# Performance work log

Hardware: AMD Instinct MI355X
Metric: run time of the kernel (lower is better)

Reference implementation:

```python
import jax, jax.numpy as jnp
import numpy as np

D = 256
N = 1024
L = 6
H = 4
NAMES = ['self', 'cross', 'self', 'cross', 'self', 'cross']


def setup_inputs() -> dict:
    key = jax.random.key(0)
    ks = jax.random.split(key, 12)
    f32 = jnp.float32
    s = D ** -0.5
    s2 = (2 * D) ** -0.5
    return {
        'desc0': jax.random.normal(ks[0], (1, D, N), f32),
        'desc1': jax.random.normal(ks[1], (1, D, N), f32),
        'desc2': jax.random.normal(ks[2], (1, D, N), f32),
        'desc3': jax.random.normal(ks[3], (1, D, N), f32),
        'dist': jax.random.uniform(ks[4], (1, N, N), f32),
        'unreachable': jnp.zeros((N, N), dtype=bool),
        'fidx': jax.random.randint(ks[5], (N, 2), 0, 100),
        'lmb': jax.random.randint(ks[6], (8, 4), 0, 100),
        'proj_w': jax.random.normal(ks[7], (3, L, 3, D, D), f32) * s,
        'proj_b': jnp.zeros((3, L, 3, D), f32),
        'merge_w': jax.random.normal(ks[8], (3, L, D, D), f32) * s,
        'merge_b': jnp.zeros((3, L, D), f32),
        'mlp_w1': jax.random.normal(ks[9], (3, L, 2 * D, 2 * D), f32) * s2,
        'mlp_b1': jnp.zeros((3, L, 2 * D), f32),
        'mlp_w2': jax.random.normal(ks[10], (3, L, D, 2 * D), f32) * s2,
        'mlp_b2': jnp.zeros((3, L, D), f32),
        'norm_g': jnp.ones((4, L, D), f32),
        'norm_b': jnp.zeros((4, L, D), f32),
    }


def _conv(w, b, x):
    # Conv1d kernel_size=1 == per-position linear over channel dim. x: [1, Cin, N]
    return jnp.einsum('od,bdn->bon', w, x) + b[None, :, None]


def _ln(x, g, b):
    # torch does LayerNorm(D) on x.transpose(1,2); equivalent to normalizing channel dim of [1, D, N]
    mu = jnp.mean(x, axis=1, keepdims=True)
    var = jnp.var(x, axis=1, keepdims=True)
    xn = (x - mu) * jax.lax.rsqrt(var + 1e-5)
    return xn * g[None, :, None] + b[None, :, None]


def _mha(pw, pb, mw, mb, q, k, v):
    # pw: [3, D, D], pb: [3, D]; q/k/v: [1, D, Nq/Nk/Nk]; mask is always None in this model
    dh = D // H
    qh = _conv(pw[0], pb[0], q).reshape(1, dh, H, -1)  # [1, dh, H, Nq]
    kh = _conv(pw[1], pb[1], k).reshape(1, dh, H, -1)
    vh = _conv(pw[2], pb[2], v).reshape(1, dh, H, -1)
    scores = jnp.einsum('bdhn,bdhm->bhnm', qh, kh) / jnp.asarray(dh, q.dtype) ** 0.5
    prob = jax.nn.softmax(scores, axis=-1)
    x = jnp.einsum('bhnm,bdhm->bdhn', prob, vh)  # [1, dh, H, Nq]
    out = _conv(mw, mb, x.reshape(1, D, -1))
    return out, scores.mean(axis=1)  # weights: [1, Nq, Nk]


def reference(desc0, desc1, desc2, desc3, dist, unreachable, fidx, lmb,
              proj_w, proj_b, merge_w, merge_b, mlp_w1, mlp_b1, mlp_w2, mlp_b2,
              norm_g, norm_b):
    # ablation == 0 path; dist, fidx, lmb feed dead code in the original forward.
    def prop(br, i, x, src):
        msg, wts = _mha(proj_w[br, i], proj_b[br, i], merge_w[br, i], merge_b[br, i], x, src, src)
        h = jnp.concatenate([x, msg], axis=1)  # [1, 2D, N]
        h = jax.nn.relu(_conv(mlp_w1[br, i], mlp_b1[br, i], h))
        return _conv(mlp_w2[br, i], mlp_b2[br, i], h), wts

    d0, d1, d2, d3 = desc0, desc1, desc2, desc3
    score1 = None
    for i, name in enumerate(NAMES):
        if name == 'cross':
            src0, src1 = d1, d0
        else:
            src0, src1 = d0, d1
        delta0, _ = prop(0, i, d0, src0)
        delta1, score1 = prop(0, i, d1, src1)
        if name == 'cross':
            delta21, _ = prop(1, i, d2, d1)
            delta12, _ = prop(1, i, d1, d2)
            d2 = _ln(d2 + delta21, norm_g[2, i], norm_b[2, i])
            delta03, _ = prop(2, i, d0, d3)
            delta30, _ = prop(2, i, d3, d0)
            d3 = _ln(d3 + delta30, norm_g[3, i], norm_b[3, i])
            d0 = d0 + delta0 + delta03
            d1 = d1 + delta1 + delta12
        else:
            delta2, _ = prop(1, i, d2, d2)
            d2 = _ln(d2 + delta2, norm_g[2, i], norm_b[2, i])
            delta3, _ = prop(2, i, d3, d3)
            d3 = _ln(d3 + delta3, norm_g[3, i], norm_b[3, i])
            d0 = d0 + delta0
            d1 = d1 + delta1
        d0 = _ln(d0, norm_g[0, i], norm_b[0, i])
        d1 = _ln(d1, norm_g[1, i], norm_b[1, i])

    scores = score1.mean(axis=1).reshape(-1)  # [N0]
    unreachable_frontiers = jnp.any(unreachable, axis=0)  # [N0]
    return jnp.where(unreachable_frontiers, jnp.asarray(-1e9, scores.dtype), scores)
```

## Files before the change

### kernel.cpp

```cpp
#include <hip/hip_runtime.h>

#define D 256
#define NPTS 1024
#define H 4
#define LNUM 6

static constexpr size_t SL = (size_t)D * NPTS;

typedef __attribute__((ext_vector_type(8))) short bf16x8;
typedef __attribute__((ext_vector_type(4))) float f32x4;

__device__ __forceinline__ unsigned f2bf(float f) {
  unsigned u = __float_as_uint(f);
  return (u + 0x7FFFu + ((u >> 16) & 1u)) >> 16;
}
__device__ __forceinline__ unsigned pack2(float a, float b) {
  return f2bf(a) | (f2bf(b) << 16);
}
__device__ __forceinline__ float bf2f(unsigned u) {
  return __uint_as_float(u << 16);
}
__device__ __forceinline__ int swz(int row, int byteInRow) {
  return row * 128 + (byteInRow ^ ((row & 7) << 4));
}

struct MMArgs {
  const unsigned short* X[18];
  const unsigned short* X2[18];
  const unsigned short* W[18];
  const float* B[18];
  void* O[18];
};

template <bool RELU>
__global__ __launch_bounds__(256) void mm_bf16(MMArgs a, int K, int xs, int os,
                                               int mode0, int qkv, int split) {
  const int z = blockIdx.z;
  const unsigned short* __restrict__ X = a.X[z];
  const unsigned short* __restrict__ X2 = a.X2[z];
  const unsigned short* __restrict__ W = a.W[z];
  const float* __restrict__ Bb = a.B[z];

  int mode = mode0, osz = os;
  if (qkv && (z % 3 == 2)) { mode = 2; osz = 1024; }

  __shared__ char sm[64 * 68 * 4];
  char* smX = sm;
  char* smW = sm + 8192;

  const int tid = threadIdx.x;
  const int n0 = blockIdx.x * 64, m0 = blockIdx.y * 64;
  const int lane = tid & 63, wid = tid >> 6;

  f32x4 acc[4] = {{0.f, 0.f, 0.f, 0.f}, {0.f, 0.f, 0.f, 0.f},
                  {0.f, 0.f, 0.f, 0.f}, {0.f, 0.f, 0.f, 0.f}};

  const int srow = tid >> 3, skb = (tid & 7) * 16;
  const int ar = wid * 16 + (lane & 15);
  const int kh = (lane >> 4) * 16;

  for (int k0 = 0; k0 < K; k0 += 64) {
    const int kw = k0 + (skb >> 1);
    int kx = kw;
    const unsigned short* xsrc = X;
    if (split && kx >= split) { xsrc = X2; kx -= split; }
#pragma unroll
    for (int p = 0; p < 2; ++p) {
      const int row = srow + 32 * p;
      *(float4*)(smX + swz(row, skb)) =
          *(const float4*)(xsrc + (size_t)(n0 + row) * xs + kx);
      *(float4*)(smW + swz(row, skb)) =
          *(const float4*)(W + (size_t)(m0 + row) * K + kw);
    }
    __syncthreads();
    const bf16x8 a0 = *(const bf16x8*)(smX + swz(ar, kh));
    const bf16x8 a1 = *(const bf16x8*)(smX + swz(ar, 64 + kh));
#pragma unroll
    for (int c = 0; c < 4; ++c) {
      const int br = c * 16 + (lane & 15);
      const bf16x8 b0 = *(const bf16x8*)(smW + swz(br, kh));
      const bf16x8 b1 = *(const bf16x8*)(smW + swz(br, 64 + kh));
      acc[c] = __builtin_amdgcn_mfma_f32_16x16x32_bf16(a0, b0, acc[c], 0, 0, 0);
      acc[c] = __builtin_amdgcn_mfma_f32_16x16x32_bf16(a1, b1, acc[c], 0, 0, 0);
    }
    __syncthreads();
  }

  float(*eps)[68] = (float(*)[68])sm;
#pragma unroll
  for (int c = 0; c < 4; ++c) {
    const float bs = Bb[m0 + c * 16 + (lane & 15)];
#pragma unroll
    for (int r = 0; r < 4; ++r) {
      float v = acc[c][r] + bs;
      if (RELU) v = fmaxf(v, 0.f);
      eps[wid * 16 + (lane >> 4) * 4 + r][c * 16 + (lane & 15)] = v;
    }
  }
  __syncthreads();

#pragma unroll
  for (int p = 0; p < 2; ++p) {
    const int row = srow + 32 * p;
    const int c0 = (tid & 7) * 8;
    if (mode == 0) {
      const float4 lo = *(const float4*)&eps[row][c0];
      const float4 hi = *(const float4*)&eps[row][c0 + 4];
      uint4 u = {pack2(lo.x, lo.y), pack2(lo.z, lo.w), pack2(hi.x, hi.y), pack2(hi.z, hi.w)};
      *(uint4*)((unsigned short*)a.O[z] + (size_t)(n0 + row) * osz + m0 + c0) = u;
    } else if (mode == 1) {
      float* O = (float*)a.O[z];
      *(float4*)(O + (size_t)(n0 + row) * osz + m0 + c0) = *(const float4*)&eps[row][c0];
      *(float4*)(O + (size_t)(n0 + row) * osz + m0 + c0 + 4) = *(const float4*)&eps[row][c0 + 4];
    } else {
      float v[8];
#pragma unroll
      for (int j = 0; j < 8; ++j) v[j] = eps[c0 + j][row];
      uint4 u = {pack2(v[0], v[1]), pack2(v[2], v[3]), pack2(v[4], v[5]), pack2(v[6], v[7])};
      *(uint4*)((unsigned short*)a.O[z] + (size_t)(m0 + row) * osz + n0 + c0) = u;
    }
  }
}

struct AttnArgs {
  const unsigned short* Q[6];
  const unsigned short* K[6];
  const unsigned short* V[6];
};

__global__ __launch_bounds__(256) void attn_split(AttnArgs a, unsigned short* part) {
  const int z = blockIdx.z;
  const int h = blockIdx.y >> 2, ck = blockIdx.y & 3;
  const int n0 = blockIdx.x * 64;
  const unsigned short* __restrict__ Qp = a.Q[z];
  const unsigned short* __restrict__ Kp = a.K[z];
  const unsigned short* __restrict__ Vp = a.V[z];

  __shared__ char sm[49152];
  char* smQ = sm;
  char* smKb = sm + 8192;
  char* smVb = sm + 24576;
  char* smP = sm + 40960;

  const int tid = threadIdx.x;
  const int lane = tid & 63, wid = tid >> 6;
  const int srow = tid >> 2, skb = (tid & 3) * 16;
  const int kb0 = ck * 256;

#pragma unroll
  for (int p = 0; p < 2; ++p) {
    const int b = skb + 64 * p;
    *(float4*)(smQ + swz(srow, b)) =
        *(const float4*)(Qp + (size_t)(n0 + srow) * 256 + h * 64 + (b >> 1));
    *(float4*)(smKb + swz(srow, b)) =
        *(const float4*)(Kp + (size_t)(kb0 + srow) * 256 + h * 64 + (b >> 1));
    *(float4*)(smVb + swz(srow, b)) =
        *(const float4*)(Vp + (size_t)(h * 64 + srow) * NPTS + kb0 + (b >> 1));
  }
  __syncthreads();

  const int ar = wid * 16 + (lane & 15);
  const int kh = (lane >> 4) * 16;
  const bf16x8 qa0 = *(const bf16x8*)(smQ + swz(ar, kh));
  const bf16x8 qa1 = *(const bf16x8*)(smQ + swz(ar, 64 + kh));

  f32x4 accO[4] = {{0.f, 0.f, 0.f, 0.f}, {0.f, 0.f, 0.f, 0.f},
                   {0.f, 0.f, 0.f, 0.f}, {0.f, 0.f, 0.f, 0.f}};
  float mrun[4] = {-1e30f, -1e30f, -1e30f, -1e30f};
  float lrun[4] = {0.f, 0.f, 0.f, 0.f};

  for (int t = 0; t < 4; ++t) {
    const int co = (t & 1) << 13;
    if (t < 3) {
      const int no = ((t + 1) & 1) << 13;
      const int kt = kb0 + (t + 1) * 64;
#pragma unroll
      for (int p = 0; p < 2; ++p) {
        const int b = skb + 64 * p;
        *(float4*)(smKb + no + swz(srow, b)) =
            *(const float4*)(Kp + (size_t)(kt + srow) * 256 + h * 64 + (b >> 1));
        *(float4*)(smVb + no + swz(srow, b)) =
            *(const float4*)(Vp + (size_t)(h * 64 + srow) * NPTS + kt + (b >> 1));
      }
    }

    f32x4 s[4];
#pragma unroll
    for (int c = 0; c < 4; ++c) {
      const int br = c * 16 + (lane & 15);
      const bf16x8 kf0 = *(const bf16x8*)(smKb + co + swz(br, kh));
      const bf16x8 kf1 = *(const bf16x8*)(smKb + co + swz(br, 64 + kh));
      f32x4 tt = {0.f, 0.f, 0.f, 0.f};
      tt = __builtin_amdgcn_mfma_f32_16x16x32_bf16(qa0, kf0, tt, 0, 0, 0);
      tt = __builtin_amdgcn_mfma_f32_16x16x32_bf16(qa1, kf1, tt, 0, 0, 0);
      s[c] = tt * 0.125f;
    }

#pragma unroll
    for (int r = 0; r < 4; ++r) {
      float mx = fmaxf(fmaxf(s[0][r], s[1][r]), fmaxf(s[2][r], s[3][r]));
#pragma unroll
      for (int o = 1; o < 16; o <<= 1) mx = fmaxf(mx, __shfl_xor(mx, o));
      const float mn = fmaxf(mrun[r], mx);
      const float corr = __expf(mrun[r] - mn);
      mrun[r] = mn;
      float ps = 0.f;
#pragma unroll
      for (int c = 0; c < 4; ++c) {
        const float e = __expf(s[c][r] - mn);
        s[c][r] = e;
        ps += e;
      }
#pragma unroll
      for (int o = 1; o < 16; o <<= 1) ps += __shfl_xor(ps, o);
      lrun[r] = lrun[r] * corr + ps;
#pragma unroll
      for (int c = 0; c < 4; ++c) accO[c][r] *= corr;
    }

#pragma unroll
    for (int c = 0; c < 4; ++c)
#pragma unroll
      for (int r = 0; r < 4; ++r) {
        const float p0 = s[c][r];
        const float p1 = __shfl_xor(p0, 1);
        if (!(lane & 1)) {
          const int row = wid * 16 + (lane >> 4) * 4 + r;
          const int ktb = (c * 16 + (lane & 15)) * 2;
          *(unsigned*)(smP + swz(row, ktb)) = pack2(p0, p1);
        }
      }

    const bf16x8 pa0 = *(const bf16x8*)(smP + swz(ar, kh));
    const bf16x8 pa1 = *(const bf16x8*)(smP + swz(ar, 64 + kh));
#pragma unroll
    for (int c = 0; c < 4; ++c) {
      const int vr = c * 16 + (lane & 15);
      const bf16x8 vb0 = *(const bf16x8*)(smVb + co + swz(vr, kh));
      const bf16x8 vb1 = *(const bf16x8*)(smVb + co + swz(vr, 64 + kh));
      accO[c] = __builtin_amdgcn_mfma_f32_16x16x32_bf16(pa0, vb0, accO[c], 0, 0, 0);
      accO[c] = __builtin_amdgcn_mfma_f32_16x16x32_bf16(pa1, vb1, accO[c], 0, 0, 0);
    }
    __syncthreads();
  }

  char* rec = (char*)part +
              (size_t)((((z * 4 + h) * 16 + blockIdx.x) * 4 + ck)) * 8704;
#pragma unroll
  for (int c = 0; c < 4; ++c)
#pragma unroll
    for (int r = 0; r < 4; ++r) {
      const float o0 = accO[c][r];
      const float o1 = __shfl_xor(o0, 1);
      if (!(lane & 1)) {
        const int row = wid * 16 + (lane >> 4) * 4 + r;
        const int col = c * 16 + (lane & 15);
        *(unsigned*)(rec + row * 128 + col * 2) = pack2(o0, o1);
      }
    }
  if ((lane & 15) == 0) {
#pragma unroll
    for (int r = 0; r < 4; ++r) {
      const int row = wid * 16 + (lane >> 4) * 4 + r;
      *(float*)(rec + 8192 + row * 4) = mrun[r];
      *(float*)(rec + 8448 + row * 4) = lrun[r];
    }
  }
}

struct CmbArgs {
  unsigned short* O[6];
};

__global__ __launch_bounds__(256) void attn_combine(CmbArgs a,
                                                    const unsigned short* part) {
  const int z = blockIdx.z, h = blockIdx.y, qb = blockIdx.x;
  const int tid = threadIdx.x;
  const int q = tid >> 2, t4 = tid & 3;
  const char* base = (const char*)part + (size_t)(((z * 4 + h) * 16 + qb) * 4) * 8704;

  float m[4], l[4];
#pragma unroll
  for (int i = 0; i < 4; ++i) {
    m[i] = *(const float*)(base + i * 8704 + 8192 + q * 4);
    l[i] = *(const float*)(base + i * 8704 + 8448 + q * 4);
  }
  const float M = fmaxf(fmaxf(m[0], m[1]), fmaxf(m[2], m[3]));
  float w[4], L = 0.f;
#pragma unroll
  for (int i = 0; i < 4; ++i) { w[i] = __expf(m[i] - M); L += w[i] * l[i]; }
  const float invL = 1.f / L;

  float o[16] = {};
#pragma unroll
  for (int i = 0; i < 4; ++i) {
    const char* Or = base + i * 8704 + q * 128 + t4 * 32;
    unsigned ua[8];
    *(uint4*)ua = *(const uint4*)Or;
    *(uint4*)(ua + 4) = *(const uint4*)(Or + 16);
#pragma unroll
    for (int j = 0; j < 8; ++j) {
      o[2 * j] += w[i] * bf2f(ua[j] & 0xFFFFu);
      o[2 * j + 1] += w[i] * bf2f(ua[j] >> 16);
    }
  }
  unsigned ou[8];
#pragma unroll
  for (int j = 0; j < 8; ++j) ou[j] = pack2(o[2 * j] * invL, o[2 * j + 1] * invL);
  unsigned short* Op = a.O[z] + (size_t)(qb * 64 + q) * 256 + h * 64 + t4 * 16;
  *(uint4*)Op = *(uint4*)ou;
  *(uint4*)(Op + 8) = *(uint4*)(ou + 4);
}

struct LnArgs {
  float* x[4];
  unsigned short* xb[4];
  const float* da[4];
  const float* db[4];
  const float* g[4];
  const float* b[4];
};

__global__ __launch_bounds__(256) void ln_rows(LnArgs a) {
  const int z = blockIdx.z;
  float* __restrict__ x = a.x[z];
  unsigned short* __restrict__ xb = a.xb[z];
  const float* __restrict__ da = a.da[z];
  const float* __restrict__ db = a.db[z];
  const float* __restrict__ g = a.g[z];
  const float* __restrict__ b = a.b[z];

  const int lane = threadIdx.x & 63, wid = threadIdx.x >> 6;
  const int n = blockIdx.x * 4 + wid;
  const size_t off = (size_t)n * 256 + lane * 4;

  float4 v = *(const float4*)(x + off);
  if (da) {
    const float4 w = *(const float4*)(da + off);
    v.x += w.x; v.y += w.y; v.z += w.z; v.w += w.w;
  }
  if (db) {
    const float4 w = *(const float4*)(db + off);
    v.x += w.x; v.y += w.y; v.z += w.z; v.w += w.w;
  }
  float s = v.x + v.y + v.z + v.w;
  float q = v.x * v.x + v.y * v.y + v.z * v.z + v.w * v.w;
#pragma unroll
  for (int o = 1; o < 64; o <<= 1) {
    s += __shfl_xor(s, o);
    q += __shfl_xor(q, o);
  }
  const float mu = s * (1.f / 256.f);
  const float var = q * (1.f / 256.f) - mu * mu;
  const float inv = rsqrtf(var + 1e-5f);
  const float4 gv = *(const float4*)(g + lane * 4);
  const float4 bv = *(const float4*)(b + lane * 4);
  float4 o;
  o.x = (v.x - mu) * inv * gv.x + bv.x;
  o.y = (v.y - mu) * inv * gv.y + bv.y;
  o.z = (v.z - mu) * inv * gv.z + bv.z;
  o.w = (v.w - mu) * inv * gv.w + bv.w;
  *(float4*)(x + off) = o;
  uint2 pk = {pack2(o.x, o.y), pack2(o.z, o.w)};
  *(uint2*)(xb + off) = pk;
}

struct TrArgs {
  const float* s[4];
  float* d[4];
  unsigned short* db[4];
};
__global__ __launch_bounds__(256) void tr_init(TrArgs a) {
  const int z = blockIdx.z;
  const int n0 = blockIdx.x * 64, c0 = blockIdx.y * 64;
  __shared__ float T[64][65];
  const int tid = threadIdx.x;
#pragma unroll
  for (int p = 0; p < 4; ++p) {
    const int row = (tid >> 4) + 16 * p;
    const int col4 = (tid & 15) * 4;
    const float4 v = *(const float4*)(a.s[z] + (size_t)(c0 + row) * NPTS + n0 + col4);
    T[row][col4] = v.x; T[row][col4 + 1] = v.y; T[row][col4 + 2] = v.z; T[row][col4 + 3] = v.w;
  }
  __syncthreads();
#pragma unroll
  for (int p = 0; p < 4; ++p) {
    const int nr = (tid >> 4) + 16 * p;
    const int c4 = (tid & 15) * 4;
    float4 v;
    v.x = T[c4][nr]; v.y = T[c4 + 1][nr]; v.z = T[c4 + 2][nr]; v.w = T[c4 + 3][nr];
    *(float4*)(a.d[z] + (size_t)(n0 + nr) * 256 + c0 + c4) = v;
    uint2 pk = {pack2(v.x, v.y), pack2(v.z, v.w)};
    *(uint2*)(a.db[z] + (size_t)(n0 + nr) * 256 + c0 + c4) = pk;
  }
}

__global__ __launch_bounds__(256) void wp_qkv(const float* __restrict__ pw,
                                              const float* __restrict__ pb,
                                              unsigned short* __restrict__ wbf,
                                              float* __restrict__ pbias) {
  const int z = blockIdx.z;
  const int pi = z / 3, j = z % 3;
  const int br = pi / 5, i = pi % 5;
  const float* src = pw + (((size_t)br * LNUM + i) * 3 + j) * 65536;
  unsigned short* dst = wbf + (size_t)pi * 655360 + (size_t)j * 65536;
  const int t = blockIdx.x * 256 + threadIdx.x;
  const int mp = t >> 6, k4 = (t & 63) * 4;
  const int m = (mp & 63) * 4 + (mp >> 6);
  const float4 v = *(const float4*)(src + (size_t)m * 256 + k4);
  uint2 pk = {pack2(v.x, v.y), pack2(v.z, v.w)};
  *(uint2*)(dst + (size_t)mp * 256 + k4) = pk;
  if (blockIdx.x == 0) {
    const float* sb = pb + (((size_t)br * LNUM + i) * 3 + j) * 256;
    const int mb = threadIdx.x;
    pbias[(size_t)z * 256 + mb] = sb[(mb & 63) * 4 + (mb >> 6)];
  }
}

__global__ __launch_bounds__(256) void wp_mw(const float* __restrict__ mw,
                                             unsigned short* __restrict__ wbf) {
  const int pi = blockIdx.z;
  const int br = pi / 5, i = pi % 5;
  const float* src = mw + ((size_t)br * LNUM + i) * 65536;
  unsigned short* dst = wbf + (size_t)pi * 655360 + 196608;
  const int t = blockIdx.x * 256 + threadIdx.x;
  const int m = t >> 6, c4 = (t & 63) * 4;
  float v[4];
#pragma unroll
  for (int u = 0; u < 4; ++u) {
    const int cp = c4 + u;
    v[u] = src[(size_t)m * 256 + (cp & 63) * 4 + (cp >> 6)];
  }
  uint2 pk = {pack2(v[0], v[1]), pack2(v[2], v[3])};
  *(uint2*)(dst + (size_t)m * 256 + c4) = pk;
}

__global__ __launch_bounds__(256) void wp_c1(const float* __restrict__ w1,
                                             unsigned short* __restrict__ wbf) {
  const int pi = blockIdx.z;
  const int br = pi / 5, i = pi % 5;
  const float* src = w1 + ((size_t)br * LNUM + i) * 262144;
  unsigned short* dst = wbf + (size_t)pi * 655360 + 262144;
  const int t = blockIdx.x * 256 + threadIdx.x;
  const float4 v = *(const float4*)(src + (size_t)t * 4);
  uint2 pk = {pack2(v.x, v.y), pack2(v.z, v.w)};
  *(uint2*)(dst + (size_t)t * 4) = pk;
}

__global__ __launch_bounds__(256) void wp_c2(const float* __restrict__ w2,
                                             unsigned short* __restrict__ wbf) {
  const int pi = blockIdx.z;
  const int br = pi / 5, i = pi % 5;
  const float* src = w2 + ((size_t)br * LNUM + i) * 131072;
  unsigned short* dst = wbf + (size_t)pi * 655360 + 524288;
  const int t = blockIdx.x * 256 + threadIdx.x;
  const float4 v = *(const float4*)(src + (size_t)t * 4);
  uint2 pk = {pack2(v.x, v.y), pack2(v.z, v.w)};
  *(uint2*)(dst + (size_t)t * 4) = pk;
}

__device__ __forceinline__ float block_reduce_sum(float v) {
  __shared__ float smr[4];
  const int lane = threadIdx.x & 63, wid = threadIdx.x >> 6;
#pragma unroll
  for (int off = 32; off; off >>= 1) v += __shfl_xor(v, off);
  if (lane == 0) smr[wid] = v;
  __syncthreads();
  if (threadIdx.x == 0) v = smr[0] + smr[1] + smr[2] + smr[3];
  return v;
}

__global__ __launch_bounds__(256) void cs1(const float* __restrict__ X,
                                           float* __restrict__ part) {
  const int r0 = blockIdx.x * 64;
  float acc = 0.f;
  for (int r = 0; r < 64; ++r) acc += X[(size_t)(r0 + r) * 256 + threadIdx.x];
  part[(size_t)blockIdx.x * 256 + threadIdx.x] = acc;
}
__global__ __launch_bounds__(256) void cs2(const float* __restrict__ part,
                                           float* __restrict__ s1) {
  float acc = 0.f;
  for (int b = 0; b < 16; ++b) acc += part[(size_t)b * 256 + threadIdx.x];
  s1[threadIdx.x] = acc;
}
__global__ __launch_bounds__(256) void matvec_qbar(const float* __restrict__ Wq,
                                                   const float* __restrict__ bq,
                                                   const float* __restrict__ s1,
                                                   float* __restrict__ qbar) {
  const int d = blockIdx.x, t = threadIdx.x;
  float s = Wq[(size_t)d * 256 + t] * s1[t];
  s = block_reduce_sum(s);
  if (t == 0) qbar[d] = s + (float)NPTS * bq[d];
}
__global__ __launch_bounds__(256) void matvec_u(const float* __restrict__ Wk,
                                                const float* __restrict__ bk,
                                                const float* __restrict__ qbar,
                                                float* __restrict__ u) {
  const int c = blockIdx.x, t = threadIdx.x;
  float s = (c < 256) ? (Wk[(size_t)t * 256 + c] * qbar[t]) : (bk[t] * qbar[t]);
  s = block_reduce_sum(s);
  if (t == 0) u[c] = s;
}

__global__ __launch_bounds__(256) void ur_or(const unsigned* __restrict__ U,
                                             unsigned* __restrict__ part) {
  const int b = blockIdx.x;
  unsigned o = 0;
  for (int r = 0; r < 16; ++r) o |= U[(size_t)(b * 16 + r) * 256 + threadIdx.x];
  part[(size_t)b * 256 + threadIdx.x] = o;
}

__global__ __launch_bounds__(256) void final2(const float* __restrict__ d0,
                                              const float* __restrict__ u,
                                              const unsigned* __restrict__ part,
                                              float* __restrict__ out) {
  const int lane = threadIdx.x & 63, wid = threadIdx.x >> 6;
  const int m = blockIdx.x * 4 + wid;
  const float4 v = *(const float4*)(d0 + (size_t)m * 256 + lane * 4);
  const float4 uu = *(const float4*)(u + lane * 4);
  float s = v.x * uu.x + v.y * uu.y + v.z * uu.z + v.w * uu.w;
  unsigned f = part[(size_t)lane * 256 + (m >> 2)];
  f = (f >> ((m & 3) * 8)) & 0xFFu;
#pragma unroll
  for (int o = 32; o; o >>= 1) {
    s += __shfl_xor(s, o);
    f |= (unsigned)__shfl_xor((int)f, o);
  }
  if (lane == 0) out[m] = f ? -1e9f : (s + u[256]) * (1.f / 32768.f);
}

extern "C" void kernel_launch(void* const* d_in, const int* in_sizes, int n_in,
                              void* d_out, int out_size, void* d_ws, size_t ws_size,
                              hipStream_t stream) {
  const float* desc[4] = {(const float*)d_in[0], (const float*)d_in[1],
                          (const float*)d_in[2], (const float*)d_in[3]};
  const unsigned char* unreach = (const unsigned char*)d_in[5];
  const float* proj_w = (const float*)d_in[8];
  const float* proj_b = (const float*)d_in[9];
  const float* merge_w = (const float*)d_in[10];
  const float* merge_b = (const float*)d_in[11];
  const float* mlp_w1 = (const float*)d_in[12];
  const float* mlp_b1 = (const float*)d_in[13];
  const float* mlp_w2 = (const float*)d_in[14];
  const float* mlp_b2 = (const float*)d_in[15];
  const float* norm_g = (const float*)d_in[16];
  const float* norm_b = (const float*)d_in[17];
  float* out = (float*)d_out;

  float* ws = (float*)d_ws;
  float* dbufF[4];
  for (int t = 0; t < 4; ++t) dbufF[t] = ws + (size_t)t * SL;
  unsigned short* dbfB[4];
  for (int t = 0; t < 4; ++t) dbfB[t] = (unsigned short*)(ws + 4 * SL) + (size_t)t * SL;
  float* deltaF[6];
  for (int p = 0; p < 6; ++p) deltaF[p] = ws + 6 * SL + (size_t)p * SL;
  unsigned short* wbf = (unsigned short*)(ws + 12 * SL);
  float* pbias = ws + 12 * SL + 4915200;
  unsigned* urpart = (unsigned*)(pbias + 11520);
  float* cspart = pbias + 11520 + 16384;
  float* s1 = cspart + 4096;
  float* qbar = s1 + 256;
  float* uvec = qbar + 256;
  unsigned short* attnpart = (unsigned short*)(ws + 12 * SL + 4915200 + 32832);
  const size_t base_f = 12 * SL + 4915200 + 32832 + 3342336;
  long long avail = (long long)(ws_size / 4) - (long long)base_f;
  const size_t SET_US = 5 * SL;
  int nsets = (int)(avail / (long long)(SET_US / 2));
  if (nsets > 6) nsets = 6;
  if (nsets < 1) nsets = 1;
  unsigned short* usBase = (unsigned short*)(ws + base_f);
  auto setQ = [&](int p) { return usBase + (size_t)p * SET_US; };
  auto setK = [&](int p) { return usBase + (size_t)p * SET_US + SL; };
  auto setV = [&](int p) { return usBase + (size_t)p * SET_US + 2 * SL; };
  auto setO = [&](int p) { return usBase + (size_t)p * SET_US + 3 * SL; };
  auto setM = [&](int p) { return usBase + (size_t)p * SET_US + 4 * SL; };
  auto setH1 = [&](int p) { return usBase + (size_t)p * SET_US; };

  ur_or<<<dim3(64), 256, 0, stream>>>((const unsigned*)unreach, urpart);
  wp_qkv<<<dim3(64, 1, 45), 256, 0, stream>>>(proj_w, proj_b, wbf, pbias);
  wp_mw<<<dim3(64, 1, 15), 256, 0, stream>>>(merge_w, wbf);
  wp_c1<<<dim3(256, 1, 15), 256, 0, stream>>>(mlp_w1, wbf);
  wp_c2<<<dim3(128, 1, 15), 256, 0, stream>>>(mlp_w2, wbf);
  {
    TrArgs ta{};
    for (int t = 0; t < 4; ++t) { ta.s[t] = desc[t]; ta.d[t] = dbufF[t]; ta.db[t] = dbfB[t]; }
    tr_init<<<dim3(16, 4, 4), 256, 0, stream>>>(ta);
  }

  static const int selfp[4][3] = {{0, 0, 0}, {0, 1, 1}, {1, 2, 2}, {2, 3, 3}};
  static const int crossp[6][3] = {{0, 0, 1}, {0, 1, 0}, {1, 2, 1},
                                   {1, 1, 2}, {2, 0, 3}, {2, 3, 0}};

  for (int i = 0; i < 5; ++i) {
    const bool cross = (i & 1);
    const int np = cross ? 6 : 4;
    const int(*props)[3] = cross ? crossp : selfp;

    for (int p0 = 0; p0 < np; p0 += nsets) {
      const int g = (np - p0 < nsets) ? (np - p0) : nsets;

      {
        MMArgs m{};
        for (int p = 0; p < g; ++p) {
          const int br = props[p0 + p][0], xi = props[p0 + p][1], si = props[p0 + p][2];
          const int pi = br * 5 + i;
          unsigned short* wb = wbf + (size_t)pi * 655360;
          const unsigned short* xq = dbfB[xi];
          const unsigned short* xsv = dbfB[si];
          m.X[p * 3 + 0] = xq; m.X2[p * 3 + 0] = xq; m.W[p * 3 + 0] = wb;
          m.B[p * 3 + 0] = pbias + ((size_t)pi * 3 + 0) * 256; m.O[p * 3 + 0] = setQ(p);
          m.X[p * 3 + 1] = xsv; m.X2[p * 3 + 1] = xsv; m.W[p * 3 + 1] = wb + 65536;
          m.B[p * 3 + 1] = pbias + ((size_t)pi * 3 + 1) * 256; m.O[p * 3 + 1] = setK(p);
          m.X[p * 3 + 2] = xsv; m.X2[p * 3 + 2] = xsv; m.W[p * 3 + 2] = wb + 131072;
          m.B[p * 3 + 2] = pbias + ((size_t)pi * 3 + 2) * 256; m.O[p * 3 + 2] = setV(p);
        }
        mm_bf16<false><<<dim3(16, 4, 3 * g), 256, 0, stream>>>(m, 256, 256, 256, 0, 1, 0);
      }
      {
        AttnArgs aa{};
        for (int p = 0; p < g; ++p) {
          aa.Q[p] = setQ(p); aa.K[p] = setK(p); aa.V[p] = setV(p);
        }
        attn_split<<<dim3(16, 16, g), 256, 0, stream>>>(aa, attnpart);
        CmbArgs cc{};
        for (int p = 0; p < g; ++p) cc.O[p] = setO(p);
        attn_combine<<<dim3(16, 4, g), 256, 0, stream>>>(cc, attnpart);
      }
      {
        MMArgs m{};
        for (int p = 0; p < g; ++p) {
          const int br = props[p0 + p][0];
          const int pi = br * 5 + i;
          m.X[p] = setO(p); m.X2[p] = setO(p);
          m.W[p] = wbf + (size_t)pi * 655360 + 196608;
          m.B[p] = merge_b + ((size_t)br * LNUM + i) * 256; m.O[p] = setM(p);
        }
        mm_bf16<false><<<dim3(16, 4, g), 256, 0, stream>>>(m, 256, 256, 256, 0, 0, 0);
      }
      {
        MMArgs m{};
        for (int p = 0; p < g; ++p) {
          const int br = props[p0 + p][0], xi = props[p0 + p][1];
          const int pi = br * 5 + i;
          m.X[p] = dbfB[xi]; m.X2[p] = setM(p);
          m.W[p] = wbf + (size_t)pi * 655360 + 262144;
          m.B[p] = mlp_b1 + ((size_t)br * LNUM + i) * 512; m.O[p] = setH1(p);
        }
        mm_bf16<true><<<dim3(16, 8, g), 256, 0, stream>>>(m, 512, 256, 512, 0, 0, 256);
      }
      {
        MMArgs m{};
        for (int p = 0; p < g; ++p) {
          const int br = props[p0 + p][0];
          const int pi = br * 5 + i;
          m.X[p] = setH1(p); m.X2[p] = setH1(p);
          m.W[p] = wbf + (size_t)pi * 655360 + 524288;
          m.B[p] = mlp_b2 + ((size_t)br * LNUM + i) * 256; m.O[p] = deltaF[p0 + p];
        }
        mm_bf16<false><<<dim3(16, 4, g), 256, 0, stream>>>(m, 512, 512, 256, 1, 0, 0);
      }
    }

    {
      LnArgs la{};
      for (int t = 0; t < 4; ++t) {
        la.x[t] = dbufF[t]; la.xb[t] = dbfB[t];
        const float* da = nullptr;
        const float* db2 = nullptr;
        for (int p = 0; p < np; ++p)
          if (props[p][1] == t) {
            if (!da) da = deltaF[p];
            else db2 = deltaF[p];
          }
        la.da[t] = da; la.db[t] = db2;
        la.g[t] = norm_g + ((size_t)t * LNUM + i) * 256;
        la.b[t] = norm_b + ((size_t)t * LNUM + i) * 256;
      }
      ln_rows<<<dim3(256, 1, 4), 256, 0, stream>>>(la);
    }
  }

  const float* Wq5 = proj_w + (((size_t)0 * LNUM + 5) * 3 + 0) * 65536;
  const float* bq5 = proj_b + (((size_t)0 * LNUM + 5) * 3 + 0) * 256;
  const float* Wk5 = proj_w + (((size_t)0 * LNUM + 5) * 3 + 1) * 65536;
  const float* bk5 = proj_b + (((size_t)0 * LNUM + 5) * 3 + 1) * 256;

  cs1<<<dim3(16), 256, 0, stream>>>(dbufF[1], cspart);
  cs2<<<dim3(1), 256, 0, stream>>>(cspart, s1);
  matvec_qbar<<<dim3(256), 256, 0, stream>>>(Wq5, bq5, s1, qbar);
  matvec_u<<<dim3(257), 256, 0, stream>>>(Wk5, bk5, qbar, uvec);
  final2<<<dim3(256), 256, 0, stream>>>(dbufF[0], uvec, urpart, out);

  (void)in_sizes; (void)n_in; (void)out_size;
}
```

Measured before the change: 388.0 us.

## Fold merge projection into MLP first layer and transpose attention score layout

The merge conv weight is pre-multiplied into the second half of the MLP first-layer weight, and the merge bias is folded into a new first-layer bias, so each propagation drops one GEMM launch and one intermediate buffer. The 1/sqrt(dh) scale moves into the Q projection epilogue. The attention kernel computes S transposed so each lane owns one query row, which removes the 16-lane shuffle reductions and the per-element shuffle when writing P. Folding the merge weights changes bf16 rounding because the fused product is itself rounded to bf16.

```diff
diff --git a/kernel.cpp b/kernel.cpp
--- a/kernel.cpp
+++ b/kernel.cpp
@@ -43,6 +43,7 @@
 
   int mode = mode0, osz = os;
   if (qkv && (z % 3 == 2)) { mode = 2; osz = 1024; }
+  const float osc = (qkv && (z % 3 == 0)) ? 0.125f : 1.0f;
 
   __shared__ char sm[64 * 68 * 4];
   char* smX = sm;
@@ -92,7 +93,7 @@
     const float bs = Bb[m0 + c * 16 + (lane & 15)];
 #pragma unroll
     for (int r = 0; r < 4; ++r) {
-      float v = acc[c][r] + bs;
+      float v = (acc[c][r] + bs) * osc;
       if (RELU) v = fmaxf(v, 0.f);
       eps[wid * 16 + (lane >> 4) * 4 + r][c * 16 + (lane & 15)] = v;
     }
@@ -159,15 +160,14 @@
   }
   __syncthreads();
 
-  const int ar = wid * 16 + (lane & 15);
   const int kh = (lane >> 4) * 16;
-  const bf16x8 qa0 = *(const bf16x8*)(smQ + swz(ar, kh));
-  const bf16x8 qa1 = *(const bf16x8*)(smQ + swz(ar, 64 + kh));
+  const int qr = wid * 16 + (lane & 15);
+  const bf16x8 qb0 = *(const bf16x8*)(smQ + swz(qr, kh));
+  const bf16x8 qb1 = *(const bf16x8*)(smQ + swz(qr, 64 + kh));
 
   f32x4 accO[4] = {{0.f, 0.f, 0.f, 0.f}, {0.f, 0.f, 0.f, 0.f},
                    {0.f, 0.f, 0.f, 0.f}, {0.f, 0.f, 0.f, 0.f}};
-  float mrun[4] = {-1e30f, -1e30f, -1e30f, -1e30f};
-  float lrun[4] = {0.f, 0.f, 0.f, 0.f};
+  float mrun = -1e30f, lrun = 0.f;
 
   for (int t = 0; t < 4; ++t) {
     const int co = (t & 1) << 13;
@@ -191,48 +191,51 @@
       const bf16x8 kf0 = *(const bf16x8*)(smKb + co + swz(br, kh));
       const bf16x8 kf1 = *(const bf16x8*)(smKb + co + swz(br, 64 + kh));
       f32x4 tt = {0.f, 0.f, 0.f, 0.f};
-      tt = __builtin_amdgcn_mfma_f32_16x16x32_bf16(qa0, kf0, tt, 0, 0, 0);
-      tt = __builtin_amdgcn_mfma_f32_16x16x32_bf16(qa1, kf1, tt, 0, 0, 0);
-      s[c] = tt * 0.125f;
-    }
-
-#pragma unroll
-    for (int r = 0; r < 4; ++r) {
-      float mx = fmaxf(fmaxf(s[0][r], s[1][r]), fmaxf(s[2][r], s[3][r]));
-#pragma unroll
-      for (int o = 1; o < 16; o <<= 1) mx = fmaxf(mx, __shfl_xor(mx, o));
-      const float mn = fmaxf(mrun[r], mx);
-      const float corr = __expf(mrun[r] - mn);
-      mrun[r] = mn;
-      float ps = 0.f;
-#pragma unroll
-      for (int c = 0; c < 4; ++c) {
+      tt = __builtin_amdgcn_mfma_f32_16x16x32_bf16(kf0, qb0, tt, 0, 0, 0);
+      tt = __builtin_amdgcn_mfma_f32_16x16x32_bf16(kf1, qb1, tt, 0, 0, 0);
+      s[c] = tt;
+    }
+
+    float mx = s[0][0];
+#pragma unroll
+    for (int c = 0; c < 4; ++c)
+#pragma unroll
+      for (int r = 0; r < 4; ++r) mx = fmaxf(mx, s[c][r]);
+    mx = fmaxf(mx, __shfl_xor(mx, 16));
+    mx = fmaxf(mx, __shfl_xor(mx, 32));
+    const float mn = fmaxf(mrun, mx);
+    const float corr = __expf(mrun - mn);
+    mrun = mn;
+    float ps = 0.f;
+#pragma unroll
+    for (int c = 0; c < 4; ++c)
+#pragma unroll
+      for (int r = 0; r < 4; ++r) {
         const float e = __expf(s[c][r] - mn);
         s[c][r] = e;
         ps += e;
       }
-#pragma unroll
-      for (int o = 1; o < 16; o <<= 1) ps += __shfl_xor(ps, o);
-      lrun[r] = lrun[r] * corr + ps;
-#pragma unroll
-      for (int c = 0; c < 4; ++c) accO[c][r] *= corr;
-    }
-
-#pragma unroll
-    for (int c = 0; c < 4; ++c)
-#pragma unroll
-      for (int r = 0; r < 4; ++r) {
-        const float p0 = s[c][r];
-        const float p1 = __shfl_xor(p0, 1);
-        if (!(lane & 1)) {
-          const int row = wid * 16 + (lane >> 4) * 4 + r;
-          const int ktb = (c * 16 + (lane & 15)) * 2;
-          *(unsigned*)(smP + swz(row, ktb)) = pack2(p0, p1);
-        }
-      }
-
-    const bf16x8 pa0 = *(const bf16x8*)(smP + swz(ar, kh));
-    const bf16x8 pa1 = *(const bf16x8*)(smP + swz(ar, 64 + kh));
+    ps += __shfl_xor(ps, 16);
+    ps += __shfl_xor(ps, 32);
+    lrun = lrun * corr + ps;
+
+#pragma unroll
+    for (int c = 0; c < 4; ++c) {
+      uint2 u;
+      u.x = pack2(s[c][0], s[c][1]);
+      u.y = pack2(s[c][2], s[c][3]);
+      *(uint2*)(smP + swz(qr, c * 32 + (lane >> 4) * 8)) = u;
+    }
+
+#pragma unroll
+    for (int r = 0; r < 4; ++r) {
+      const float cr = __shfl(corr, ((lane >> 4) & 3) * 4 + r);
+#pragma unroll
+      for (int c = 0; c < 4; ++c) accO[c][r] *= cr;
+    }
+
+    const bf16x8 pa0 = *(const bf16x8*)(smP + swz(qr, kh));
+    const bf16x8 pa1 = *(const bf16x8*)(smP + swz(qr, 64 + kh));
 #pragma unroll
     for (int c = 0; c < 4; ++c) {
       const int vr = c * 16 + (lane & 15);
@@ -258,13 +261,9 @@
         *(unsigned*)(rec + row * 128 + col * 2) = pack2(o0, o1);
       }
     }
-  if ((lane & 15) == 0) {
-#pragma unroll
-    for (int r = 0; r < 4; ++r) {
-      const int row = wid * 16 + (lane >> 4) * 4 + r;
-      *(float*)(rec + 8192 + row * 4) = mrun[r];
-      *(float*)(rec + 8448 + row * 4) = lrun[r];
-    }
+  if (lane < 16) {
+    *(float*)(rec + 8192 + (wid * 16 + lane) * 4) = mrun;
+    *(float*)(rec + 8448 + (wid * 16 + lane) * 4) = lrun;
   }
 }
 
@@ -417,26 +416,27 @@
   }
 }
 
-__global__ __launch_bounds__(256) void wp_mw(const float* __restrict__ mw,
-                                             unsigned short* __restrict__ wbf) {
+__global__ __launch_bounds__(256) void wp_mwt(const float* __restrict__ mw,
+                                              unsigned short* __restrict__ wbf,
+                                              float* __restrict__ zb) {
   const int pi = blockIdx.z;
   const int br = pi / 5, i = pi % 5;
   const float* src = mw + ((size_t)br * LNUM + i) * 65536;
   unsigned short* dst = wbf + (size_t)pi * 655360 + 196608;
   const int t = blockIdx.x * 256 + threadIdx.x;
-  const int m = t >> 6, c4 = (t & 63) * 4;
+  const int cp = t >> 6, m4 = (t & 63) * 4;
+  const int c = (cp & 63) * 4 + (cp >> 6);
   float v[4];
 #pragma unroll
-  for (int u = 0; u < 4; ++u) {
-    const int cp = c4 + u;
-    v[u] = src[(size_t)m * 256 + (cp & 63) * 4 + (cp >> 6)];
-  }
+  for (int u = 0; u < 4; ++u) v[u] = src[(size_t)(m4 + u) * 256 + c];
   uint2 pk = {pack2(v[0], v[1]), pack2(v[2], v[3])};
-  *(uint2*)(dst + (size_t)m * 256 + c4) = pk;
+  *(uint2*)(dst + (size_t)cp * 256 + m4) = pk;
+  if (blockIdx.x == 0 && pi == 0) zb[threadIdx.x] = 0.f;
 }
 
 __global__ __launch_bounds__(256) void wp_c1(const float* __restrict__ w1,
-                                             unsigned short* __restrict__ wbf) {
+                                             unsigned short* __restrict__ wbf,
+                                             unsigned short* __restrict__ whi) {
   const int pi = blockIdx.z;
   const int br = pi / 5, i = pi % 5;
   const float* src = w1 + ((size_t)br * LNUM + i) * 262144;
@@ -445,6 +445,9 @@
   const float4 v = *(const float4*)(src + (size_t)t * 4);
   uint2 pk = {pack2(v.x, v.y), pack2(v.z, v.w)};
   *(uint2*)(dst + (size_t)t * 4) = pk;
+  const int idx = t * 4, row = idx >> 9, col = idx & 511;
+  if (col >= 256)
+    *(uint2*)(whi + (size_t)pi * 131072 + (size_t)row * 256 + (col - 256)) = pk;
 }
 
 __global__ __launch_bounds__(256) void wp_c2(const float* __restrict__ w2,
@@ -457,6 +460,27 @@
   const float4 v = *(const float4*)(src + (size_t)t * 4);
   uint2 pk = {pack2(v.x, v.y), pack2(v.z, v.w)};
   *(uint2*)(dst + (size_t)t * 4) = pk;
+}
+
+__global__ __launch_bounds__(256) void b1fold(const float* __restrict__ w1,
+                                              const float* __restrict__ mb,
+                                              const float* __restrict__ b1,
+                                              float* __restrict__ out) {
+  const int pi = blockIdx.z;
+  const int br = pi / 5, i = pi % 5;
+  const float* Wp = w1 + ((size_t)br * LNUM + i) * 262144;
+  const float* Bp = mb + ((size_t)br * LNUM + i) * 256;
+  const float* b1s = b1 + ((size_t)br * LNUM + i) * 512;
+  __shared__ float mbs[256];
+  mbs[threadIdx.x] = Bp[threadIdx.x];
+  __syncthreads();
+  for (int o = threadIdx.x; o < 512; o += 256) {
+    float s = b1s[o];
+    const float* Wr = Wp + (size_t)o * 512 + 256;
+#pragma unroll 4
+    for (int m = 0; m < 256; ++m) s = fmaf(Wr[m], mbs[m], s);
+    out[(size_t)pi * 512 + o] = s;
+  }
 }
 
 __device__ __forceinline__ float block_reduce_sum(float v) {
@@ -561,10 +585,13 @@
   float* s1 = cspart + 4096;
   float* qbar = s1 + 256;
   float* uvec = qbar + 256;
-  unsigned short* attnpart = (unsigned short*)(ws + 12 * SL + 4915200 + 32832);
-  const size_t base_f = 12 * SL + 4915200 + 32832 + 3342336;
+  float* b1prime = uvec + 260;
+  float* zbias = b1prime + 7680;
+  unsigned short* attnpart = (unsigned short*)(ws + 12 * SL + 4915200 + 40960);
+  unsigned short* whi = attnpart + (size_t)2 * 3342336;
+  const size_t base_f = 12 * SL + 4915200 + 40960 + 3342336 + 983040;
   long long avail = (long long)(ws_size / 4) - (long long)base_f;
-  const size_t SET_US = 5 * SL;
+  const size_t SET_US = 4 * SL;
   int nsets = (int)(avail / (long long)(SET_US / 2));
   if (nsets > 6) nsets = 6;
   if (nsets < 1) nsets = 1;
@@ -573,14 +600,25 @@
   auto setK = [&](int p) { return usBase + (size_t)p * SET_US + SL; };
   auto setV = [&](int p) { return usBase + (size_t)p * SET_US + 2 * SL; };
   auto setO = [&](int p) { return usBase + (size_t)p * SET_US + 3 * SL; };
-  auto setM = [&](int p) { return usBase + (size_t)p * SET_US + 4 * SL; };
   auto setH1 = [&](int p) { return usBase + (size_t)p * SET_US; };
 
   ur_or<<<dim3(64), 256, 0, stream>>>((const unsigned*)unreach, urpart);
   wp_qkv<<<dim3(64, 1, 45), 256, 0, stream>>>(proj_w, proj_b, wbf, pbias);
-  wp_mw<<<dim3(64, 1, 15), 256, 0, stream>>>(merge_w, wbf);
-  wp_c1<<<dim3(256, 1, 15), 256, 0, stream>>>(mlp_w1, wbf);
+  wp_mwt<<<dim3(64, 1, 15), 256, 0, stream>>>(merge_w, wbf, zbias);
+  wp_c1<<<dim3(256, 1, 15), 256, 0, stream>>>(mlp_w1, wbf, whi);
   wp_c2<<<dim3(128, 1, 15), 256, 0, stream>>>(mlp_w2, wbf);
+  b1fold<<<dim3(1, 1, 15), 256, 0, stream>>>(mlp_w1, merge_b, mlp_b1, b1prime);
+  {
+    MMArgs m{};
+    for (int pi = 0; pi < 15; ++pi) {
+      const unsigned short* xw = whi + (size_t)pi * 131072;
+      m.X[pi] = xw; m.X2[pi] = xw;
+      m.W[pi] = wbf + (size_t)pi * 655360 + 196608;
+      m.B[pi] = zbias;
+      m.O[pi] = wbf + (size_t)pi * 655360 + 262144 + 256;
+    }
+    mm_bf16<false><<<dim3(8, 4, 15), 256, 0, stream>>>(m, 256, 256, 512, 0, 0, 0);
+  }
   {
     TrArgs ta{};
     for (int t = 0; t < 4; ++t) { ta.s[t] = desc[t]; ta.d[t] = dbufF[t]; ta.db[t] = dbfB[t]; }
@@ -629,22 +667,11 @@
       {
         MMArgs m{};
         for (int p = 0; p < g; ++p) {
-          const int br = props[p0 + p][0];
-          const int pi = br * 5 + i;
-          m.X[p] = setO(p); m.X2[p] = setO(p);
-          m.W[p] = wbf + (size_t)pi * 655360 + 196608;
-          m.B[p] = merge_b + ((size_t)br * LNUM + i) * 256; m.O[p] = setM(p);
-        }
-        mm_bf16<false><<<dim3(16, 4, g), 256, 0, stream>>>(m, 256, 256, 256, 0, 0, 0);
-      }
-      {
-        MMArgs m{};
-        for (int p = 0; p < g; ++p) {
           const int br = props[p0 + p][0], xi = props[p0 + p][1];
           const int pi = br * 5 + i;
-          m.X[p] = dbfB[xi]; m.X2[p] = setM(p);
+          m.X[p] = dbfB[xi]; m.X2[p] = setO(p);
           m.W[p] = wbf + (size_t)pi * 655360 + 262144;
-          m.B[p] = mlp_b1 + ((size_t)br * LNUM + i) * 512; m.O[p] = setH1(p);
+          m.B[p] = b1prime + (size_t)pi * 512; m.O[p] = setH1(p);
         }
         mm_bf16<true><<<dim3(16, 8, g), 256, 0, stream>>>(m, 512, 256, 512, 0, 0, 256);
       }
```

After: 328.2 us, median of 2. 1.18x faster.
